# Kernel optimization log

Hardware: AMD Instinct MI355X
Metric: run time of the kernel (lower is better)

## Reference

```python
import jax, jax.numpy as jnp
import numpy as np

EMBED_DIM = 1024
NUM_HEADS = 16
HEAD_DIM = EMBED_DIM // NUM_HEADS


def setup_inputs() -> dict:
    key = jax.random.key(0)
    ks = jax.random.split(key, 9)
    B, S, E = 4, 2048, EMBED_DIM
    scale = 1.0 / np.sqrt(E)
    x = jax.random.normal(ks[0], (B, S, E), dtype=jnp.float32)
    # Linear layers: weight [E, E] (out, in) and bias [E], torch-style init scale
    Wq = jax.random.uniform(ks[1], (E, E), jnp.float32, -scale, scale)
    bq = jax.random.uniform(ks[2], (E,), jnp.float32, -scale, scale)
    Wk = jax.random.uniform(ks[3], (E, E), jnp.float32, -scale, scale)
    bk = jax.random.uniform(ks[4], (E,), jnp.float32, -scale, scale)
    Wv = jax.random.uniform(ks[5], (E, E), jnp.float32, -scale, scale)
    bv = jax.random.uniform(ks[6], (E,), jnp.float32, -scale, scale)
    Wo = jax.random.uniform(ks[7], (E, E), jnp.float32, -scale, scale)
    bo = jax.random.uniform(ks[8], (E,), jnp.float32, -scale, scale)
    return {"x": x, "Wq": Wq, "bq": bq, "Wk": Wk, "bk": bk,
            "Wv": Wv, "bv": bv, "Wo": Wo, "bo": bo}


def reference(x, Wq, bq, Wk, bk, Wv, bv, Wo, bo):
    B, S, E = x.shape
    H, D = NUM_HEADS, HEAD_DIM

    def proj(W, b):
        # torch Linear: x @ W.T + b ; reshape to [B, H, S, D]
        y = jnp.einsum('bse,fe->bsf', x, W) + b
        return y.reshape(B, S, H, D).transpose(0, 2, 1, 3)

    Q = proj(Wq, bq)
    K = proj(Wk, bk)
    V = proj(Wv, bv)
    scores = jnp.einsum('bhqd,bhkd->bhqk', Q, K) / jnp.sqrt(
        jnp.asarray(D, dtype=jnp.float32))
    attn = jax.nn.softmax(scores, axis=-1)
    out = jnp.einsum('bhqk,bhkd->bhqd', attn, V)
    out = out.transpose(0, 2, 1, 3).reshape(B, S, E)
    out = jnp.einsum('bse,fe->bsf', out, Wo) + bo
    return out
```

## Files before the change

### kernel.cpp

```cpp
#include <hip/hip_runtime.h>
#include <math.h>

#define SEQ 2048
#define EMB 1024
#define NH 16
#define HD 64
#define BATCH 4
#define MROWS (BATCH * SEQ)

typedef unsigned short u16;
typedef unsigned int u32;
typedef _Float16 f16;
using half8   = __attribute__((ext_vector_type(8))) f16;
using fp16x2  = __attribute__((ext_vector_type(2))) __fp16;
using vfloat4 = __attribute__((ext_vector_type(4))) float;

__device__ __forceinline__ u16 f2h(float f) {
    union { f16 h; u16 u; } x; x.h = (f16)f; return x.u;
}
__device__ __forceinline__ u32 pk2h(float a, float b) {
    union { fp16x2 h; u32 u; } x;
    x.h = __builtin_amdgcn_cvt_pkrtz(a, b);
    return x.u;
}
__device__ __forceinline__ float exp2v(float x) {
    float r; asm("v_exp_f32 %0, %1" : "=v"(r) : "v"(x)); return r;
}

__device__ __forceinline__ void gload16(const void* g, void* l) {
    __builtin_amdgcn_global_load_lds(
        (const __attribute__((address_space(1))) void*)g,
        (__attribute__((address_space(3))) void*)l, 16, 0, 0);
}

__global__ __launch_bounds__(256) void cvt5_kernel(
    const float* __restrict__ x,  const float* __restrict__ wq,
    const float* __restrict__ wk, const float* __restrict__ wv,
    const float* __restrict__ wo,
    uint2* __restrict__ xh, uint2* __restrict__ wqkv, uint2* __restrict__ woh)
{
    int gid = blockIdx.x * 256 + threadIdx.x;
    const float4* src; uint2* dst; int o;
    if (gid < (1 << 21)) {
        src = (const float4*)x; dst = xh; o = gid;
    } else {
        int g = gid - (1 << 21);
        int r = g >> 18;
        o = g & ((1 << 18) - 1);
        if      (r == 0) { src = (const float4*)wq; dst = wqkv; }
        else if (r == 1) { src = (const float4*)wk; dst = wqkv + (1 << 18); }
        else if (r == 2) { src = (const float4*)wv; dst = wqkv + (2 << 18); }
        else             { src = (const float4*)wo; dst = woh; }
    }
    float4 v = src[o];
    dst[o] = make_uint2(pk2h(v.x, v.y), pk2h(v.z, v.w));
}

__global__ __launch_bounds__(256) void gemm_qkv_kernel(
    const u16* __restrict__ A, const u16* __restrict__ Wqkv,
    const float* __restrict__ bq, const float* __restrict__ bk,
    const float* __restrict__ bv,
    u16* __restrict__ Qo, u16* __restrict__ Ko, u16* __restrict__ Vo,
    float sq)
{
    __shared__ char lds[16384];
    char* As = lds;
    char* Bs = lds + 8192;
    const int tid = threadIdx.x, wave = tid >> 6, lane = tid & 63;
    const int bm = blockIdx.y, bn = blockIdx.x;
    const int mat = bn >> 3;
    const int wr = wave >> 1, wc = wave & 1;

    const int srow  = wave * 16 + (lane >> 2);
    const int sslot = lane & 3;
    const int ldso  = wave * 1024 + (lane << 4);
    const u16* Ab = A    + (size_t)bm * 128 * EMB;
    const u16* Wb = Wqkv + (size_t)bn * 128 * EMB;

    vfloat4 acc[4][4] = {};

    for (int k0 = 0; k0 < EMB; k0 += 32) {
        __syncthreads();
        #pragma unroll
        for (int i2 = 0; i2 < 2; ++i2) {
            int row = i2 * 64 + srow;
            int ko  = ((sslot ^ ((row >> 1) & 3)) << 3);
            gload16(Ab + (size_t)row * EMB + k0 + ko, As + i2 * 4096 + ldso);
            gload16(Wb + (size_t)row * EMB + k0 + ko, Bs + i2 * 4096 + ldso);
        }
        __syncthreads();

        half8 af[4], bfr[4];
        #pragma unroll
        for (int m = 0; m < 4; ++m) {
            int r = wr * 64 + m * 16 + (lane & 15);
            af[m] = *(const half8*)(As + r * 64 + ((((lane >> 4) ^ ((r >> 1) & 3)) << 4)));
        }
        #pragma unroll
        for (int n = 0; n < 4; ++n) {
            int r = wc * 64 + n * 16 + (lane & 15);
            bfr[n] = *(const half8*)(Bs + r * 64 + ((((lane >> 4) ^ ((r >> 1) & 3)) << 4)));
        }
        #pragma unroll
        for (int m = 0; m < 4; ++m)
            #pragma unroll
            for (int n = 0; n < 4; ++n)
                acc[m][n] = __builtin_amdgcn_mfma_f32_16x16x32_f16(af[m], bfr[n], acc[m][n], 0, 0, 0);
    }

    const float* bp = (mat == 0) ? bq : ((mat == 1) ? bk : bv);
    const float scale = (mat == 0) ? sq : 1.0f;
    u16* Co = (mat == 0) ? Qo : ((mat == 1) ? Ko : Vo);
    const int row0 = bm * 128 + wr * 64;
    const int col0 = (bn & 7) * 128 + wc * 64;

    #pragma unroll
    for (int n = 0; n < 4; ++n) {
        int col = col0 + n * 16 + (lane & 15);
        float bb = bp[col];
        int h = col >> 6, d = col & 63;
        #pragma unroll
        for (int m = 0; m < 4; ++m)
            #pragma unroll
            for (int j = 0; j < 4; ++j) {
                int row = row0 + m * 16 + (lane >> 4) * 4 + j;
                int b = row >> 11, s = row & (SEQ - 1);
                float val = (acc[m][n][j] + bb) * scale;
                if (mat != 2) {
                    Co[(((size_t)(b * NH + h)) * SEQ + s) * HD + d] = f2h(val);
                } else {
                    Co[(((size_t)(b * NH + h)) * HD + d) * SEQ + s] = f2h(val);
                }
            }
    }
}

__global__ __launch_bounds__(256) void gemm_f16_kernel(
    const u16* __restrict__ A, const u16* __restrict__ W,
    const float* __restrict__ bias, float* __restrict__ C)
{
    __shared__ char lds[16384];
    char* As = lds;
    char* Bs = lds + 8192;
    const int tid = threadIdx.x, wave = tid >> 6, lane = tid & 63;
    const int bm = blockIdx.y, bn = blockIdx.x;
    const int wr = wave >> 1, wc = wave & 1;

    const int srow  = wave * 16 + (lane >> 2);
    const int sslot = lane & 3;
    const int ldso  = wave * 1024 + (lane << 4);
    const u16* Ab = A + (size_t)bm * 128 * EMB;
    const u16* Wb = W + (size_t)bn * 128 * EMB;

    vfloat4 acc[4][4] = {};

    for (int k0 = 0; k0 < EMB; k0 += 32) {
        __syncthreads();
        #pragma unroll
        for (int i2 = 0; i2 < 2; ++i2) {
            int row = i2 * 64 + srow;
            int ko  = ((sslot ^ ((row >> 1) & 3)) << 3);
            gload16(Ab + (size_t)row * EMB + k0 + ko, As + i2 * 4096 + ldso);
            gload16(Wb + (size_t)row * EMB + k0 + ko, Bs + i2 * 4096 + ldso);
        }
        __syncthreads();

        half8 af[4], bfr[4];
        #pragma unroll
        for (int m = 0; m < 4; ++m) {
            int r = wr * 64 + m * 16 + (lane & 15);
            af[m] = *(const half8*)(As + r * 64 + ((((lane >> 4) ^ ((r >> 1) & 3)) << 4)));
        }
        #pragma unroll
        for (int n = 0; n < 4; ++n) {
            int r = wc * 64 + n * 16 + (lane & 15);
            bfr[n] = *(const half8*)(Bs + r * 64 + ((((lane >> 4) ^ ((r >> 1) & 3)) << 4)));
        }
        #pragma unroll
        for (int m = 0; m < 4; ++m)
            #pragma unroll
            for (int n = 0; n < 4; ++n)
                acc[m][n] = __builtin_amdgcn_mfma_f32_16x16x32_f16(af[m], bfr[n], acc[m][n], 0, 0, 0);
    }

    const int row0 = bm * 128 + wr * 64, col0 = bn * 128 + wc * 64;
    #pragma unroll
    for (int n = 0; n < 4; ++n) {
        int col = col0 + n * 16 + (lane & 15);
        float bb = bias[col];
        #pragma unroll
        for (int m = 0; m < 4; ++m)
            #pragma unroll
            for (int j = 0; j < 4; ++j) {
                int row = row0 + m * 16 + (lane >> 4) * 4 + j;
                C[(size_t)row * EMB + col] = acc[m][n][j] + bb;
            }
    }
}

__device__ __forceinline__ void stage_rows(const u16* g, int rstride, char* dst,
                                           int wave, int lane) {
    int r = wave * 8 + (lane >> 3), sl = lane & 7;
    #pragma unroll
    for (int i2 = 0; i2 < 2; ++i2) {
        int row = i2 * 32 + r;
        gload16(g + (size_t)row * rstride + ((sl ^ (row & 7)) << 3),
                dst + i2 * 4096 + wave * 1024 + (lane << 4));
    }
}

__global__ __launch_bounds__(256) void attn_kernel(
    const u16* __restrict__ Q, const u16* __restrict__ K,
    const u16* __restrict__ Vt, u16* __restrict__ O)
{
    __shared__ char lds[40960];
    char* QPs = lds;
    char* Kb0 = lds + 8192;
    char* Kb1 = lds + 16384;
    char* Vb0 = lds + 24576;
    char* Vb1 = lds + 32768;

    const int tid = threadIdx.x, wave = tid >> 6, lane = tid & 63;
    const int c = lane >> 4, li = lane & 15;

    const int swz = (blockIdx.x & 7) * 128 + (blockIdx.x >> 3);
    const int bh = swz >> 4;
    const int q0 = (swz & 15) << 7;

    const u16* Qg = Q  + ((size_t)bh * SEQ + q0) * HD;
    const u16* Kg = K  + (size_t)bh * SEQ * HD;
    const u16* Vg = Vt + (size_t)bh * HD * SEQ;

    stage_rows(Qg, HD, QPs, wave, lane);
    stage_rows(Kg, HD, Kb0, wave, lane);
    stage_rows(Vg, SEQ, Vb0, wave, lane);
    __syncthreads();

    half8 qf[2][2];
    const int q = wave * 16 + li;
    #pragma unroll
    for (int cc = 0; cc < 2; ++cc)
        qf[0][cc] = *(const half8*)(QPs + q * 128 + (((4 * cc + c) ^ (q & 7)) << 4));
    __syncthreads();
    stage_rows(Qg + (size_t)64 * HD, HD, QPs, wave, lane);
    __syncthreads();
    #pragma unroll
    for (int cc = 0; cc < 2; ++cc)
        qf[1][cc] = *(const half8*)(QPs + q * 128 + (((4 * cc + c) ^ (q & 7)) << 4));

    const half8 ones8 = {1, 1, 1, 1, 1, 1, 1, 1};
    char* Pw = QPs + wave * 2048;
    vfloat4 o0[4] = {}, o1[4] = {};
    vfloat4 l0 = {}, l1 = {};

    for (int kt = 0; kt < SEQ / 64; ++kt) {
        char* Kc = (kt & 1) ? Kb1 : Kb0;
        char* Vc = (kt & 1) ? Vb1 : Vb0;
        if (kt < SEQ / 64 - 1) {
            stage_rows(Kg + (size_t)(kt + 1) * 64 * HD, HD,
                       (kt & 1) ? Kb0 : Kb1, wave, lane);
            stage_rows(Vg + (kt + 1) * 64, SEQ,
                       (kt & 1) ? Vb0 : Vb1, wave, lane);
        }

        vfloat4 s0[4] = {}, s1[4] = {};
        #pragma unroll
        for (int n = 0; n < 4; ++n) {
            int key = 16 * n + li;
            #pragma unroll
            for (int cc = 0; cc < 2; ++cc) {
                half8 kb = *(const half8*)(Kc + key * 128 + (((4 * cc + c) ^ (li & 7)) << 4));
                s0[n] = __builtin_amdgcn_mfma_f32_16x16x32_f16(kb, qf[0][cc], s0[n], 0, 0, 0);
                s1[n] = __builtin_amdgcn_mfma_f32_16x16x32_f16(kb, qf[1][cc], s1[n], 0, 0, 0);
            }
        }

        #pragma unroll
        for (int n = 0; n < 4; ++n)
            #pragma unroll
            for (int j = 0; j < 4; ++j) {
                s0[n][j] = exp2v(s0[n][j]);
                s1[n][j] = exp2v(s1[n][j]);
            }

        half8 pf0[2], pf1[2];
        #pragma unroll
        for (int n = 0; n < 4; ++n) {
            u32 w0 = pk2h(s0[n][0], s0[n][1]);
            u32 w1 = pk2h(s0[n][2], s0[n][3]);
            *(uint2*)(Pw + li * 128 + (((2 * n + (c >> 1)) ^ (li & 7)) << 4) + ((c & 1) << 3))
                = make_uint2(w0, w1);
        }
        #pragma unroll
        for (int cc = 0; cc < 2; ++cc)
            pf0[cc] = *(const half8*)(Pw + li * 128 + (((4 * cc + c) ^ (li & 7)) << 4));
        #pragma unroll
        for (int n = 0; n < 4; ++n) {
            u32 w0 = pk2h(s1[n][0], s1[n][1]);
            u32 w1 = pk2h(s1[n][2], s1[n][3]);
            *(uint2*)(Pw + li * 128 + (((2 * n + (c >> 1)) ^ (li & 7)) << 4) + ((c & 1) << 3))
                = make_uint2(w0, w1);
        }
        #pragma unroll
        for (int cc = 0; cc < 2; ++cc)
            pf1[cc] = *(const half8*)(Pw + li * 128 + (((4 * cc + c) ^ (li & 7)) << 4));

        #pragma unroll
        for (int n = 0; n < 4; ++n) {
            int r = 16 * n + li;
            #pragma unroll
            for (int cc = 0; cc < 2; ++cc) {
                half8 vf = *(const half8*)(Vc + r * 128 + (((4 * cc + c) ^ (li & 7)) << 4));
                o0[n] = __builtin_amdgcn_mfma_f32_16x16x32_f16(vf, pf0[cc], o0[n], 0, 0, 0);
                o1[n] = __builtin_amdgcn_mfma_f32_16x16x32_f16(vf, pf1[cc], o1[n], 0, 0, 0);
            }
        }
        #pragma unroll
        for (int cc = 0; cc < 2; ++cc) {
            l0 = __builtin_amdgcn_mfma_f32_16x16x32_f16(ones8, pf0[cc], l0, 0, 0, 0);
            l1 = __builtin_amdgcn_mfma_f32_16x16x32_f16(ones8, pf1[cc], l1, 0, 0, 0);
        }

        __syncthreads();
    }

    const int b = bh >> 4, h = bh & 15;
    const size_t r0 = ((size_t)b * SEQ + q0 + wave * 16 + li) * EMB + h * 64;
    const size_t r1 = ((size_t)b * SEQ + q0 + 64 + wave * 16 + li) * EMB + h * 64;
    float i0 = 1.0f / l0[0];
    float i1 = 1.0f / l1[0];
    #pragma unroll
    for (int n = 0; n < 4; ++n) {
        *(uint2*)(O + r0 + 16 * n + 4 * c) =
            make_uint2(pk2h(o0[n][0] * i0, o0[n][1] * i0),
                       pk2h(o0[n][2] * i0, o0[n][3] * i0));
        *(uint2*)(O + r1 + 16 * n + 4 * c) =
            make_uint2(pk2h(o1[n][0] * i1, o1[n][1] * i1),
                       pk2h(o1[n][2] * i1, o1[n][3] * i1));
    }
}

extern "C" void kernel_launch(void* const* d_in, const int* in_sizes, int n_in,
                              void* d_out, int out_size, void* d_ws, size_t ws_size,
                              hipStream_t stream) {
    const float* x  = (const float*)d_in[0];
    const float* Wq = (const float*)d_in[1];
    const float* bq = (const float*)d_in[2];
    const float* Wk = (const float*)d_in[3];
    const float* bk = (const float*)d_in[4];
    const float* Wv = (const float*)d_in[5];
    const float* bv = (const float*)d_in[6];
    const float* Wo = (const float*)d_in[7];
    const float* bo = (const float*)d_in[8];
    float* out = (float*)d_out;

    char* ws = (char*)d_ws;
    u16* xh   = (u16*)(ws);
    u16* Qh   = (u16*)(ws + ((size_t)16 << 20));
    u16* Kh   = (u16*)(ws + ((size_t)32 << 20));
    u16* Vh   = (u16*)(ws + ((size_t)48 << 20));
    u16* Ah   = (u16*)(ws + ((size_t)64 << 20));
    u16* Wqkv = (u16*)(ws + ((size_t)80 << 20));
    u16* Woh  = (u16*)(ws + ((size_t)88 << 20));

    const int nCvt = (1 << 21) + (1 << 20);

    cvt5_kernel<<<nCvt / 256, 256, 0, stream>>>(
        x, Wq, Wk, Wv, Wo, (uint2*)xh, (uint2*)Wqkv, (uint2*)Woh);

    const float SCALE_Q = 0.125f * 1.4426950408889634f;
    gemm_qkv_kernel<<<dim3(3 * EMB / 128, MROWS / 128), 256, 0, stream>>>(
        xh, Wqkv, bq, bk, bv, Qh, Kh, Vh, SCALE_Q);

    attn_kernel<<<dim3(SEQ / 128 * BATCH * NH), 256, 0, stream>>>(Qh, Kh, Vh, Ah);

    gemm_f16_kernel<<<dim3(EMB / 128, MROWS / 128), 256, 0, stream>>>(Ah, Woh, bo, out);
}
```

Before: 231.6 us.

## Double-buffer LDS in projection GEMMs, vectorize V store, add MFMA priority hints

```diff
diff --git a/kernel.cpp b/kernel.cpp
--- a/kernel.cpp
+++ b/kernel.cpp
@@ -63,9 +63,7 @@
     u16* __restrict__ Qo, u16* __restrict__ Ko, u16* __restrict__ Vo,
     float sq)
 {
-    __shared__ char lds[16384];
-    char* As = lds;
-    char* Bs = lds + 8192;
+    __shared__ char lds[32768];
     const int tid = threadIdx.x, wave = tid >> 6, lane = tid & 63;
     const int bm = blockIdx.y, bn = blockIdx.x;
     const int mat = bn >> 3;
@@ -79,17 +77,28 @@
 
     vfloat4 acc[4][4] = {};
 
-    for (int k0 = 0; k0 < EMB; k0 += 32) {
-        __syncthreads();
-        #pragma unroll
-        for (int i2 = 0; i2 < 2; ++i2) {
-            int row = i2 * 64 + srow;
-            int ko  = ((sslot ^ ((row >> 1) & 3)) << 3);
-            gload16(Ab + (size_t)row * EMB + k0 + ko, As + i2 * 4096 + ldso);
-            gload16(Wb + (size_t)row * EMB + k0 + ko, Bs + i2 * 4096 + ldso);
-        }
-        __syncthreads();
-
+#define QKV_STAGE(k0, bufi)                                                   \
+    {                                                                         \
+        char* Ad = lds + (bufi) * 16384;                                      \
+        char* Bd = Ad + 8192;                                                 \
+        _Pragma("unroll")                                                     \
+        for (int i2 = 0; i2 < 2; ++i2) {                                      \
+            int row = i2 * 64 + srow;                                         \
+            int ko  = ((sslot ^ ((row >> 1) & 3)) << 3);                      \
+            gload16(Ab + (size_t)row * EMB + (k0) + ko, Ad + i2 * 4096 + ldso); \
+            gload16(Wb + (size_t)row * EMB + (k0) + ko, Bd + i2 * 4096 + ldso); \
+        }                                                                     \
+    }
+
+    QKV_STAGE(0, 0);
+    __syncthreads();
+
+    for (int it = 0; it < EMB / 32; ++it) {
+        const int cur = it & 1;
+        if (it + 1 < EMB / 32) QKV_STAGE((it + 1) * 32, cur ^ 1);
+
+        char* As = lds + cur * 16384;
+        char* Bs = As + 8192;
         half8 af[4], bfr[4];
         #pragma unroll
         for (int m = 0; m < 4; ++m) {
@@ -106,7 +115,10 @@
             #pragma unroll
             for (int n = 0; n < 4; ++n)
                 acc[m][n] = __builtin_amdgcn_mfma_f32_16x16x32_f16(af[m], bfr[n], acc[m][n], 0, 0, 0);
-    }
+
+        __syncthreads();
+    }
+#undef QKV_STAGE
 
     const float* bp = (mat == 0) ? bq : ((mat == 1) ? bk : bv);
     const float scale = (mat == 0) ? sq : 1.0f;
@@ -119,19 +131,27 @@
         int col = col0 + n * 16 + (lane & 15);
         float bb = bp[col];
         int h = col >> 6, d = col & 63;
-        #pragma unroll
-        for (int m = 0; m < 4; ++m)
-            #pragma unroll
-            for (int j = 0; j < 4; ++j) {
-                int row = row0 + m * 16 + (lane >> 4) * 4 + j;
+        if (mat != 2) {
+            #pragma unroll
+            for (int m = 0; m < 4; ++m)
+                #pragma unroll
+                for (int j = 0; j < 4; ++j) {
+                    int row = row0 + m * 16 + (lane >> 4) * 4 + j;
+                    int b = row >> 11, s = row & (SEQ - 1);
+                    Co[(((size_t)(b * NH + h)) * SEQ + s) * HD + d] =
+                        f2h((acc[m][n][j] + bb) * scale);
+                }
+        } else {
+            #pragma unroll
+            for (int m = 0; m < 4; ++m) {
+                int row = row0 + m * 16 + (lane >> 4) * 4;
                 int b = row >> 11, s = row & (SEQ - 1);
-                float val = (acc[m][n][j] + bb) * scale;
-                if (mat != 2) {
-                    Co[(((size_t)(b * NH + h)) * SEQ + s) * HD + d] = f2h(val);
-                } else {
-                    Co[(((size_t)(b * NH + h)) * HD + d) * SEQ + s] = f2h(val);
-                }
+                u32 w0 = pk2h(acc[m][n][0] + bb, acc[m][n][1] + bb);
+                u32 w1 = pk2h(acc[m][n][2] + bb, acc[m][n][3] + bb);
+                *(uint2*)(Co + (((size_t)(b * NH + h)) * HD + d) * SEQ + s) =
+                    make_uint2(w0, w1);
             }
+        }
     }
 }
 
@@ -139,9 +159,7 @@
     const u16* __restrict__ A, const u16* __restrict__ W,
     const float* __restrict__ bias, float* __restrict__ C)
 {
-    __shared__ char lds[16384];
-    char* As = lds;
-    char* Bs = lds + 8192;
+    __shared__ char lds[32768];
     const int tid = threadIdx.x, wave = tid >> 6, lane = tid & 63;
     const int bm = blockIdx.y, bn = blockIdx.x;
     const int wr = wave >> 1, wc = wave & 1;
@@ -154,17 +172,28 @@
 
     vfloat4 acc[4][4] = {};
 
-    for (int k0 = 0; k0 < EMB; k0 += 32) {
-        __syncthreads();
-        #pragma unroll
-        for (int i2 = 0; i2 < 2; ++i2) {
-            int row = i2 * 64 + srow;
-            int ko  = ((sslot ^ ((row >> 1) & 3)) << 3);
-            gload16(Ab + (size_t)row * EMB + k0 + ko, As + i2 * 4096 + ldso);
-            gload16(Wb + (size_t)row * EMB + k0 + ko, Bs + i2 * 4096 + ldso);
-        }
-        __syncthreads();
-
+#define F16_STAGE(k0, bufi)                                                   \
+    {                                                                         \
+        char* Ad = lds + (bufi) * 16384;                                      \
+        char* Bd = Ad + 8192;                                                 \
+        _Pragma("unroll")                                                     \
+        for (int i2 = 0; i2 < 2; ++i2) {                                      \
+            int row = i2 * 64 + srow;                                         \
+            int ko  = ((sslot ^ ((row >> 1) & 3)) << 3);                      \
+            gload16(Ab + (size_t)row * EMB + (k0) + ko, Ad + i2 * 4096 + ldso); \
+            gload16(Wb + (size_t)row * EMB + (k0) + ko, Bd + i2 * 4096 + ldso); \
+        }                                                                     \
+    }
+
+    F16_STAGE(0, 0);
+    __syncthreads();
+
+    for (int it = 0; it < EMB / 32; ++it) {
+        const int cur = it & 1;
+        if (it + 1 < EMB / 32) F16_STAGE((it + 1) * 32, cur ^ 1);
+
+        char* As = lds + cur * 16384;
+        char* Bs = As + 8192;
         half8 af[4], bfr[4];
         #pragma unroll
         for (int m = 0; m < 4; ++m) {
@@ -181,7 +210,10 @@
             #pragma unroll
             for (int n = 0; n < 4; ++n)
                 acc[m][n] = __builtin_amdgcn_mfma_f32_16x16x32_f16(af[m], bfr[n], acc[m][n], 0, 0, 0);
-    }
+
+        __syncthreads();
+    }
+#undef F16_STAGE
 
     const int row0 = bm * 128 + wr * 64, col0 = bn * 128 + wc * 64;
     #pragma unroll
@@ -264,6 +296,7 @@
         }
 
         vfloat4 s0[4] = {}, s1[4] = {};
+        __builtin_amdgcn_s_setprio(1);
         #pragma unroll
         for (int n = 0; n < 4; ++n) {
             int key = 16 * n + li;
@@ -274,6 +307,7 @@
                 s1[n] = __builtin_amdgcn_mfma_f32_16x16x32_f16(kb, qf[1][cc], s1[n], 0, 0, 0);
             }
         }
+        __builtin_amdgcn_s_setprio(0);
 
         #pragma unroll
         for (int n = 0; n < 4; ++n)
@@ -305,6 +339,7 @@
         for (int cc = 0; cc < 2; ++cc)
             pf1[cc] = *(const half8*)(Pw + li * 128 + (((4 * cc + c) ^ (li & 7)) << 4));
 
+        __builtin_amdgcn_s_setprio(1);
         #pragma unroll
         for (int n = 0; n < 4; ++n) {
             int r = 16 * n + li;
@@ -320,6 +355,7 @@
             l0 = __builtin_amdgcn_mfma_f32_16x16x32_f16(ones8, pf0[cc], l0, 0, 0, 0);
             l1 = __builtin_amdgcn_mfma_f32_16x16x32_f16(ones8, pf1[cc], l1, 0, 0, 0);
         }
+        __builtin_amdgcn_s_setprio(0);
 
         __syncthreads();
     }
```

After: 214.6 us, median of 2. 1.08x faster.
